# Kernel tuning notes

Hardware: AMD Instinct MI355X
Metric: run time of the kernel (lower is better)

Reference implementation:

```python
import jax, jax.numpy as jnp
import numpy as np

HEAD_SIZE = 128  # embeddings_dims // no_of_heads = 4096 // 32


def apply_rope(v):
    # v: [B, S, d] with d = HEAD_SIZE; interleaved-pair rotation as in source
    B, S, d = v.shape
    pos = jnp.arange(S, dtype=jnp.float32)[:, None]              # [S, 1]
    idx = jnp.arange(0, d, 2, dtype=jnp.float32)[None, :]        # [1, d//2]
    theta = jnp.power(10000.0, -2.0 * idx / d)                   # [1, d//2]
    angles = pos * theta                                         # [S, d//2]
    cos = jnp.cos(angles)
    sin = jnp.sin(angles)
    vr = v.reshape(B, S, d // 2, 2)
    x0, x1 = vr[..., 0], vr[..., 1]
    out = jnp.stack([x0 * cos - x1 * sin, x1 * cos + x0 * sin], axis=-1)
    return out.reshape(B, S, d)


def setup_inputs() -> dict:
    key = jax.random.key(0)
    kx, kq, kk, kv = jax.random.split(key, 4)
    B, S, D = 2, 4096, 4096
    d = HEAD_SIZE
    scale = 1.0 / np.sqrt(D)
    return {
        "x": jax.random.normal(kx, (B, S, D), dtype=jnp.float32),
        "Wq": jax.random.normal(kq, (d, D), dtype=jnp.float32) * scale,
        "Wk": jax.random.normal(kk, (d, D), dtype=jnp.float32) * scale,
        "Wv": jax.random.normal(kv, (d, D), dtype=jnp.float32) * scale,
    }


def reference(x, Wq, Wk, Wv):
    # single attention head, non-flash path (eval mode: dropout = identity)
    B, S, D = x.shape
    q = jnp.einsum('bsd,hd->bsh', x, Wq)  # [B, S, head]
    k = jnp.einsum('bsd,hd->bsh', x, Wk)
    v = jnp.einsum('bsd,hd->bsh', x, Wv)
    q = apply_rope(q)
    k = apply_rope(k)
    scale = k.shape[-1] ** (-0.5)
    scores = jnp.einsum('bqh,bkh->bqk', q, k) * scale  # [B, S, S]
    causal = jnp.tril(jnp.ones((S, S), dtype=bool))
    scores = jnp.where(causal, scores, -jnp.inf)
    weights = jax.nn.softmax(scores, axis=-1)
    out = jnp.einsum('bqk,bkh->bqh', weights, v)  # [B, S, head]
    return out
```

## Files before the change

### kernel.cpp

```cpp
#include <hip/hip_runtime.h>

typedef _Float16 half8 __attribute__((ext_vector_type(8)));
typedef _Float16 half2v __attribute__((ext_vector_type(2)));
typedef float f32x4 __attribute__((ext_vector_type(4)));

#define S_LEN 4096
#define D_DIM 4096
#define HD 128


#define ASTR 40
#define QSTR 136
__global__ __launch_bounds__(256) void proj_kernel(const float* __restrict__ x,
                                                   const float* __restrict__ wq,
                                                   const float* __restrict__ wk,
                                                   const float* __restrict__ wv,
                                                   _Float16* __restrict__ qw,
                                                   _Float16* __restrict__ kw,
                                                   _Float16* __restrict__ vt) {
    __shared__ __align__(16) _Float16 smem[128 * QSTR];
    _Float16* Ash = smem;
    _Float16* Bsh = smem + 128 * ASTR;
    const int tid = threadIdx.x;
    const int bx = blockIdx.x;
    const int M0 = blockIdx.y * 128;
    const float* w = (bx == 0) ? wq : (bx == 1) ? wk : wv;
    const int lane = tid & 63, wid = tid >> 6;
    const int wr = wid >> 1, wc = wid & 1;
    const int l15 = lane & 15, quad = lane >> 4;

    const int srow = tid >> 1, scol = (tid & 1) * 16;
    const float* xa = x + (size_t)(M0 + srow) * D_DIM + scol;
    const float* wb = w + (size_t)srow * D_DIM + scol;
    _Float16* ash = &Ash[srow * ASTR + scol];
    _Float16* bsh = &Bsh[srow * ASTR + scol];

    f32x4 acc[4][4];
    for (int mi = 0; mi < 4; ++mi)
        for (int ni = 0; ni < 4; ++ni)
            acc[mi][ni] = (f32x4){0.f, 0.f, 0.f, 0.f};

    float4 a0 = *(const float4*)(xa);
    float4 a1 = *(const float4*)(xa + 4);
    float4 a2 = *(const float4*)(xa + 8);
    float4 a3 = *(const float4*)(xa + 12);
    float4 b0 = *(const float4*)(wb);
    float4 b1 = *(const float4*)(wb + 4);
    float4 b2 = *(const float4*)(wb + 8);
    float4 b3 = *(const float4*)(wb + 12);

    for (int k0 = 0; k0 < D_DIM; k0 += 32) {
        half8 ha0 = { (_Float16)a0.x, (_Float16)a0.y, (_Float16)a0.z, (_Float16)a0.w,
                      (_Float16)a1.x, (_Float16)a1.y, (_Float16)a1.z, (_Float16)a1.w };
        half8 ha1 = { (_Float16)a2.x, (_Float16)a2.y, (_Float16)a2.z, (_Float16)a2.w,
                      (_Float16)a3.x, (_Float16)a3.y, (_Float16)a3.z, (_Float16)a3.w };
        half8 hb0 = { (_Float16)b0.x, (_Float16)b0.y, (_Float16)b0.z, (_Float16)b0.w,
                      (_Float16)b1.x, (_Float16)b1.y, (_Float16)b1.z, (_Float16)b1.w };
        half8 hb1 = { (_Float16)b2.x, (_Float16)b2.y, (_Float16)b2.z, (_Float16)b2.w,
                      (_Float16)b3.x, (_Float16)b3.y, (_Float16)b3.z, (_Float16)b3.w };
        *(half8*)ash = ha0;
        *(half8*)(ash + 8) = ha1;
        *(half8*)bsh = hb0;
        *(half8*)(bsh + 8) = hb1;
        __syncthreads();
        if (k0 + 32 < D_DIM) {
            a0 = *(const float4*)(xa + k0 + 32);
            a1 = *(const float4*)(xa + k0 + 36);
            a2 = *(const float4*)(xa + k0 + 40);
            a3 = *(const float4*)(xa + k0 + 44);
            b0 = *(const float4*)(wb + k0 + 32);
            b1 = *(const float4*)(wb + k0 + 36);
            b2 = *(const float4*)(wb + k0 + 40);
            b3 = *(const float4*)(wb + k0 + 44);
        }
        half8 af[4], bf[4];
        for (int mi = 0; mi < 4; ++mi)
            af[mi] = *(const half8*)&Ash[(wr * 64 + mi * 16 + l15) * ASTR + quad * 8];
        for (int ni = 0; ni < 4; ++ni)
            bf[ni] = *(const half8*)&Bsh[(wc * 64 + ni * 16 + l15) * ASTR + quad * 8];
        for (int mi = 0; mi < 4; ++mi)
            for (int ni = 0; ni < 4; ++ni)
                acc[mi][ni] = __builtin_amdgcn_mfma_f32_16x16x32_f16(af[mi], bf[ni],
                                                                     acc[mi][ni], 0, 0, 0);
        __syncthreads();
    }

    if (bx < 2) {
        for (int mi = 0; mi < 4; ++mi)
            for (int ni = 0; ni < 4; ++ni)
                for (int r = 0; r < 4; ++r)
                    smem[(wr * 64 + mi * 16 + quad * 4 + r) * QSTR +
                         wc * 64 + ni * 16 + l15] = (_Float16)acc[mi][ni][r];
        __syncthreads();
        _Float16* dst = ((bx == 0) ? qw : kw) + (size_t)M0 * HD;
        const int row = tid >> 1, c0 = (tid & 1) * 64;
        for (int j = 0; j < 8; ++j)
            *(half8*)&dst[row * HD + c0 + j * 8] = *(const half8*)&smem[row * QSTR + c0 + j * 8];
    } else {
        for (int mi = 0; mi < 4; ++mi)
            for (int ni = 0; ni < 4; ++ni)
                for (int r = 0; r < 4; ++r)
                    smem[(wc * 64 + ni * 16 + l15) * QSTR +
                         wr * 64 + mi * 16 + quad * 4 + r] = (_Float16)acc[mi][ni][r];
        __syncthreads();
        _Float16* dst = vt + (size_t)(M0 >> 12) * HD * S_LEN + (M0 & (S_LEN - 1));
        const int hd = tid >> 1, c0 = (tid & 1) * 64;
        for (int j = 0; j < 8; ++j)
            *(half8*)&dst[(size_t)hd * S_LEN + c0 + j * 8] =
                *(const half8*)&smem[hd * QSTR + c0 + j * 8];
    }
}

__global__ __launch_bounds__(256) void rope_kernel(_Float16* __restrict__ qw,
                                                   _Float16* __restrict__ kw) {
    const int g = blockIdx.x * 256 + threadIdx.x;
    const int m = g >> 6, p = g & 63;
    const int s = m & (S_LEN - 1);
    const float theta = exp2f((float)p * -0.4152410118609203f);
    float sn, cn;
    sincosf((float)s * theta, &sn, &cn);
    const size_t off = (size_t)m * HD + 2 * p;
    half2v qv = *(half2v*)&qw[off];
    half2v kv = *(half2v*)&kw[off];
    float q0 = qv[0], q1 = qv[1], k0 = kv[0], k1 = kv[1];
    half2v qo = { (_Float16)(q0 * cn - q1 * sn), (_Float16)(q1 * cn + q0 * sn) };
    half2v ko = { (_Float16)(k0 * cn - k1 * sn), (_Float16)(k1 * cn + k0 * sn) };
    *(half2v*)&qw[off] = qo;
    *(half2v*)&kw[off] = ko;
}

template<bool MASKED>
__device__ __forceinline__ void attn_tile(int kbase, int qg, int l15, int quad,
                                          const _Float16* __restrict__ kb,
                                          const _Float16* __restrict__ vtb,
                                          const half8* bq, f32x4* acc,
                                          float& mrun, float& lrun) {
    const float csc = 0.1275174348796053f;
    const _Float16* kr = kb + (size_t)(kbase + l15) * HD + quad * 8;
    f32x4 st0 = (f32x4){0.f, 0.f, 0.f, 0.f};
    f32x4 st1 = (f32x4){0.f, 0.f, 0.f, 0.f};
    for (int kk = 0; kk < 4; ++kk) {
        half8 k0 = *(const half8*)(kr + kk * 32);
        half8 k1 = *(const half8*)(kr + 16 * HD + kk * 32);
        st0 = __builtin_amdgcn_mfma_f32_16x16x32_f16(k0, bq[kk], st0, 0, 0, 0);
        st1 = __builtin_amdgcn_mfma_f32_16x16x32_f16(k1, bq[kk], st1, 0, 0, 0);
    }
    half8 va[8];
    const _Float16* vr = vtb + (size_t)l15 * S_LEN + kbase + quad * 8;
    for (int c = 0; c < 8; ++c)
        va[c] = *(const half8*)(vr + (size_t)c * 16 * S_LEN);
    float p0[4], p1[4];
    float mloc = -1e30f;
    for (int r = 0; r < 4; ++r) {
        float v0 = st0[r] * csc;
        float v1 = st1[r] * csc;
        if (MASKED) {
            const int key0 = kbase + quad * 4 + r;
            if (key0 > qg)      v0 = -1e30f;
            if (key0 + 16 > qg) v1 = -1e30f;
        }
        p0[r] = v0; p1[r] = v1;
        mloc = fmaxf(mloc, fmaxf(v0, v1));
    }
    mloc = fmaxf(mloc, __shfl_xor(mloc, 16));
    mloc = fmaxf(mloc, __shfl_xor(mloc, 32));
    const float mnew = fmaxf(mrun, mloc);
    const float alpha = exp2f(mrun - mnew);
    mrun = mnew;
    float ls = 0.f;
    for (int r = 0; r < 4; ++r) {
        p0[r] = exp2f(p0[r] - mnew);
        p1[r] = exp2f(p1[r] - mnew);
        ls += p0[r] + p1[r];
    }
    ls += __shfl_xor(ls, 16);
    ls += __shfl_xor(ls, 32);
    lrun = lrun * alpha + ls;
    for (int c = 0; c < 8; ++c)
        acc[c] *= alpha;
    int ph0 = __builtin_bit_cast(int, __builtin_amdgcn_cvt_pkrtz(p0[0], p0[1]));
    int ph1 = __builtin_bit_cast(int, __builtin_amdgcn_cvt_pkrtz(p0[2], p0[3]));
    int ph2 = __builtin_bit_cast(int, __builtin_amdgcn_cvt_pkrtz(p1[0], p1[1]));
    int ph3 = __builtin_bit_cast(int, __builtin_amdgcn_cvt_pkrtz(p1[2], p1[3]));
    const int s0 = (l15 + (((quad << 1)    ) & 3) * 16) * 4;
    const int s1 = (l15 + (((quad << 1) + 1) & 3) * 16) * 4;
    int a0 = __builtin_amdgcn_ds_bpermute(s0, ph0);
    int a1 = __builtin_amdgcn_ds_bpermute(s0, ph1);
    int a2 = __builtin_amdgcn_ds_bpermute(s1, ph0);
    int a3 = __builtin_amdgcn_ds_bpermute(s1, ph1);
    int b0 = __builtin_amdgcn_ds_bpermute(s0, ph2);
    int b1 = __builtin_amdgcn_ds_bpermute(s0, ph3);
    int b2 = __builtin_amdgcn_ds_bpermute(s1, ph2);
    int b3 = __builtin_amdgcn_ds_bpermute(s1, ph3);
    const bool lo = quad < 2;
    int4 pi = { lo ? a0 : b0, lo ? a1 : b1, lo ? a2 : b2, lo ? a3 : b3 };
    half8 pf = __builtin_bit_cast(half8, pi);
    for (int c = 0; c < 8; ++c)
        acc[c] = __builtin_amdgcn_mfma_f32_16x16x32_f16(va[c], pf, acc[c], 0, 0, 0);
}

__global__ __launch_bounds__(256) void attn_kernel(const _Float16* __restrict__ q,
                                                   const _Float16* __restrict__ k,
                                                   const _Float16* __restrict__ vt,
                                                   float* __restrict__ out) {
    __shared__ __align__(16) float Osh[4][16][132];
    __shared__ float msh[4][16];
    __shared__ float lsh[4][16];
    const int tid = threadIdx.x;
    const int lane = tid & 63, wv_ = tid >> 6;
    const int l15 = lane & 15, quad = lane >> 4;
    const int bidx = blockIdx.x;
    const int b = bidx & 1;
    const int t = 255 - (bidx >> 1);
    const int qb = t * 16;
    const int qg = qb + l15;

    const _Float16* qp = q + (size_t)(b * S_LEN + qb) * HD;
    half8 bq[4];
    for (int kk = 0; kk < 4; ++kk)
        bq[kk] = *(const half8*)&qp[l15 * HD + kk * 32 + quad * 8];

    f32x4 acc[8];
    for (int c = 0; c < 8; ++c) acc[c] = (f32x4){0.f, 0.f, 0.f, 0.f};
    float mrun = -1e30f, lrun = 0.f;

    const _Float16* kb = k + (size_t)b * S_LEN * HD;
    const _Float16* vtb = vt + (size_t)b * HD * S_LEN;

    const int nfull = (qb + 1) >> 5;
    for (int kt = wv_; kt < nfull; kt += 4)
        attn_tile<false>(kt * 32, qg, l15, quad, kb, vtb, bq, acc, mrun, lrun);
    if ((nfull & 3) == wv_)
        attn_tile<true>(nfull * 32, qg, l15, quad, kb, vtb, bq, acc, mrun, lrun);

    for (int c = 0; c < 8; ++c)
        *(f32x4*)&Osh[wv_][l15][c * 16 + quad * 4] = acc[c];
    if (quad == 0) { msh[wv_][l15] = mrun; lsh[wv_][l15] = lrun; }
    __syncthreads();

    const int qr = tid >> 4, dg = (tid & 15) * 8;
    float m0 = msh[0][qr], m1 = msh[1][qr], m2 = msh[2][qr], m3 = msh[3][qr];
    float mm = fmaxf(fmaxf(m0, m1), fmaxf(m2, m3));
    float f0 = exp2f(m0 - mm), f1 = exp2f(m1 - mm), f2 = exp2f(m2 - mm), f3 = exp2f(m3 - mm);
    float l = lsh[0][qr] * f0 + lsh[1][qr] * f1 + lsh[2][qr] * f2 + lsh[3][qr] * f3;
    f32x4 oa = (f32x4){0.f, 0.f, 0.f, 0.f}, ob = oa;
    oa += *(f32x4*)&Osh[0][qr][dg] * f0;  ob += *(f32x4*)&Osh[0][qr][dg + 4] * f0;
    oa += *(f32x4*)&Osh[1][qr][dg] * f1;  ob += *(f32x4*)&Osh[1][qr][dg + 4] * f1;
    oa += *(f32x4*)&Osh[2][qr][dg] * f2;  ob += *(f32x4*)&Osh[2][qr][dg + 4] * f2;
    oa += *(f32x4*)&Osh[3][qr][dg] * f3;  ob += *(f32x4*)&Osh[3][qr][dg + 4] * f3;
    const float inv = 1.0f / l;
    float* op = out + (size_t)(b * S_LEN + qb + qr) * HD + dg;
    *(float4*)op       = (float4){oa[0] * inv, oa[1] * inv, oa[2] * inv, oa[3] * inv};
    *(float4*)(op + 4) = (float4){ob[0] * inv, ob[1] * inv, ob[2] * inv, ob[3] * inv};
}

extern "C" void kernel_launch(void* const* d_in, const int* in_sizes, int n_in,
                              void* d_out, int out_size, void* d_ws, size_t ws_size,
                              hipStream_t stream) {
    const float* x  = (const float*)d_in[0];
    const float* Wq = (const float*)d_in[1];
    const float* Wk = (const float*)d_in[2];
    const float* Wv = (const float*)d_in[3];
    float* out = (float*)d_out;
    char* ws = (char*)d_ws;
    _Float16* qw = (_Float16*)(ws);
    _Float16* kw = (_Float16*)(ws + (2u << 20));
    _Float16* vt = (_Float16*)(ws + (4u << 20));

    proj_kernel<<<dim3(3, 64), dim3(256), 0, stream>>>(x, Wq, Wk, Wv, qw, kw, vt);
    rope_kernel<<<dim3(2048), dim3(256), 0, stream>>>(qw, kw);
    attn_kernel<<<dim3(512), dim3(256), 0, stream>>>(qw, kw, vt, out);
}
```

Baseline: 399.3 us.

## Halve projection M-tile, double-buffer its LDS, and prefetch K fragments in attention

```diff
diff --git a/kernel.cpp b/kernel.cpp
--- a/kernel.cpp
+++ b/kernel.cpp
@@ -18,96 +18,87 @@
                                                    _Float16* __restrict__ qw,
                                                    _Float16* __restrict__ kw,
                                                    _Float16* __restrict__ vt) {
-    __shared__ __align__(16) _Float16 smem[128 * QSTR];
-    _Float16* Ash = smem;
-    _Float16* Bsh = smem + 128 * ASTR;
+    __shared__ __align__(16) _Float16 smem[17408];
     const int tid = threadIdx.x;
     const int bx = blockIdx.x;
-    const int M0 = blockIdx.y * 128;
+    const int M0 = blockIdx.y * 64;
     const float* w = (bx == 0) ? wq : (bx == 1) ? wk : wv;
-    const int lane = tid & 63, wid = tid >> 6;
-    const int wr = wid >> 1, wc = wid & 1;
+    const int lane = tid & 63, wv_ = tid >> 6;
     const int l15 = lane & 15, quad = lane >> 4;
 
-    const int srow = tid >> 1, scol = (tid & 1) * 16;
-    const float* xa = x + (size_t)(M0 + srow) * D_DIM + scol;
-    const float* wb = w + (size_t)srow * D_DIM + scol;
-    _Float16* ash = &Ash[srow * ASTR + scol];
-    _Float16* bsh = &Bsh[srow * ASTR + scol];
-
-    f32x4 acc[4][4];
+    const int arow = tid >> 2, acol = (tid & 3) * 8;
+    const int brow = tid >> 1, bcol = (tid & 1) * 16;
+    const float* xa = x + (size_t)(M0 + arow) * D_DIM + acol;
+    const float* wb = w + (size_t)brow * D_DIM + bcol;
+
+    f32x4 acc[4][2];
     for (int mi = 0; mi < 4; ++mi)
-        for (int ni = 0; ni < 4; ++ni)
+        for (int ni = 0; ni < 2; ++ni)
             acc[mi][ni] = (f32x4){0.f, 0.f, 0.f, 0.f};
 
-    float4 a0 = *(const float4*)(xa);
-    float4 a1 = *(const float4*)(xa + 4);
-    float4 a2 = *(const float4*)(xa + 8);
-    float4 a3 = *(const float4*)(xa + 12);
-    float4 b0 = *(const float4*)(wb);
-    float4 b1 = *(const float4*)(wb + 4);
-    float4 b2 = *(const float4*)(wb + 8);
-    float4 b3 = *(const float4*)(wb + 12);
-
-    for (int k0 = 0; k0 < D_DIM; k0 += 32) {
-        half8 ha0 = { (_Float16)a0.x, (_Float16)a0.y, (_Float16)a0.z, (_Float16)a0.w,
-                      (_Float16)a1.x, (_Float16)a1.y, (_Float16)a1.z, (_Float16)a1.w };
-        half8 ha1 = { (_Float16)a2.x, (_Float16)a2.y, (_Float16)a2.z, (_Float16)a2.w,
-                      (_Float16)a3.x, (_Float16)a3.y, (_Float16)a3.z, (_Float16)a3.w };
-        half8 hb0 = { (_Float16)b0.x, (_Float16)b0.y, (_Float16)b0.z, (_Float16)b0.w,
-                      (_Float16)b1.x, (_Float16)b1.y, (_Float16)b1.z, (_Float16)b1.w };
-        half8 hb1 = { (_Float16)b2.x, (_Float16)b2.y, (_Float16)b2.z, (_Float16)b2.w,
-                      (_Float16)b3.x, (_Float16)b3.y, (_Float16)b3.z, (_Float16)b3.w };
-        *(half8*)ash = ha0;
-        *(half8*)(ash + 8) = ha1;
-        *(half8*)bsh = hb0;
-        *(half8*)(bsh + 8) = hb1;
+    float4 pa[2][2], pb[2][4];
+    pa[0][0] = *(const float4*)(xa);      pa[0][1] = *(const float4*)(xa + 4);
+    pb[0][0] = *(const float4*)(wb);      pb[0][1] = *(const float4*)(wb + 4);
+    pb[0][2] = *(const float4*)(wb + 8);  pb[0][3] = *(const float4*)(wb + 12);
+    pa[1][0] = *(const float4*)(xa + 32); pa[1][1] = *(const float4*)(xa + 36);
+    pb[1][0] = *(const float4*)(wb + 32); pb[1][1] = *(const float4*)(wb + 36);
+    pb[1][2] = *(const float4*)(wb + 40); pb[1][3] = *(const float4*)(wb + 44);
+
+    for (int i = 0; i < 128; ++i) {
+        const int p = i & 1;
+        _Float16* Ash = smem + p * 7680;
+        _Float16* Bsh = smem + p * 7680 + 2560;
+        half8 ha = { (_Float16)pa[p][0].x, (_Float16)pa[p][0].y, (_Float16)pa[p][0].z, (_Float16)pa[p][0].w,
+                     (_Float16)pa[p][1].x, (_Float16)pa[p][1].y, (_Float16)pa[p][1].z, (_Float16)pa[p][1].w };
+        half8 hb0 = { (_Float16)pb[p][0].x, (_Float16)pb[p][0].y, (_Float16)pb[p][0].z, (_Float16)pb[p][0].w,
+                      (_Float16)pb[p][1].x, (_Float16)pb[p][1].y, (_Float16)pb[p][1].z, (_Float16)pb[p][1].w };
+        half8 hb1 = { (_Float16)pb[p][2].x, (_Float16)pb[p][2].y, (_Float16)pb[p][2].z, (_Float16)pb[p][2].w,
+                      (_Float16)pb[p][3].x, (_Float16)pb[p][3].y, (_Float16)pb[p][3].z, (_Float16)pb[p][3].w };
+        *(half8*)&Ash[arow * ASTR + acol] = ha;
+        *(half8*)&Bsh[brow * ASTR + bcol] = hb0;
+        *(half8*)&Bsh[brow * ASTR + bcol + 8] = hb1;
+        if (i + 2 < 128) {
+            const int off = (i + 2) * 32;
+            pa[p][0] = *(const float4*)(xa + off);      pa[p][1] = *(const float4*)(xa + off + 4);
+            pb[p][0] = *(const float4*)(wb + off);      pb[p][1] = *(const float4*)(wb + off + 4);
+            pb[p][2] = *(const float4*)(wb + off + 8);  pb[p][3] = *(const float4*)(wb + off + 12);
+        }
         __syncthreads();
-        if (k0 + 32 < D_DIM) {
-            a0 = *(const float4*)(xa + k0 + 32);
-            a1 = *(const float4*)(xa + k0 + 36);
-            a2 = *(const float4*)(xa + k0 + 40);
-            a3 = *(const float4*)(xa + k0 + 44);
-            b0 = *(const float4*)(wb + k0 + 32);
-            b1 = *(const float4*)(wb + k0 + 36);
-            b2 = *(const float4*)(wb + k0 + 40);
-            b3 = *(const float4*)(wb + k0 + 44);
-        }
-        half8 af[4], bf[4];
-        for (int mi = 0; mi < 4; ++mi)
-            af[mi] = *(const half8*)&Ash[(wr * 64 + mi * 16 + l15) * ASTR + quad * 8];
-        for (int ni = 0; ni < 4; ++ni)
-            bf[ni] = *(const half8*)&Bsh[(wc * 64 + ni * 16 + l15) * ASTR + quad * 8];
-        for (int mi = 0; mi < 4; ++mi)
-            for (int ni = 0; ni < 4; ++ni)
+        half8 af[4], bf[2];
+        for (int mi = 0; mi < 4; ++mi)
+            af[mi] = *(const half8*)&Ash[(mi * 16 + l15) * ASTR + quad * 8];
+        for (int ni = 0; ni < 2; ++ni)
+            bf[ni] = *(const half8*)&Bsh[(wv_ * 32 + ni * 16 + l15) * ASTR + quad * 8];
+        for (int mi = 0; mi < 4; ++mi)
+            for (int ni = 0; ni < 2; ++ni)
                 acc[mi][ni] = __builtin_amdgcn_mfma_f32_16x16x32_f16(af[mi], bf[ni],
                                                                      acc[mi][ni], 0, 0, 0);
-        __syncthreads();
-    }
+    }
+    __syncthreads();
 
     if (bx < 2) {
         for (int mi = 0; mi < 4; ++mi)
-            for (int ni = 0; ni < 4; ++ni)
+            for (int ni = 0; ni < 2; ++ni)
                 for (int r = 0; r < 4; ++r)
-                    smem[(wr * 64 + mi * 16 + quad * 4 + r) * QSTR +
-                         wc * 64 + ni * 16 + l15] = (_Float16)acc[mi][ni][r];
+                    smem[(mi * 16 + quad * 4 + r) * QSTR + wv_ * 32 + ni * 16 + l15] =
+                        (_Float16)acc[mi][ni][r];
         __syncthreads();
         _Float16* dst = ((bx == 0) ? qw : kw) + (size_t)M0 * HD;
-        const int row = tid >> 1, c0 = (tid & 1) * 64;
-        for (int j = 0; j < 8; ++j)
+        const int row = tid >> 2, c0 = (tid & 3) * 32;
+        for (int j = 0; j < 4; ++j)
             *(half8*)&dst[row * HD + c0 + j * 8] = *(const half8*)&smem[row * QSTR + c0 + j * 8];
     } else {
         for (int mi = 0; mi < 4; ++mi)
-            for (int ni = 0; ni < 4; ++ni)
+            for (int ni = 0; ni < 2; ++ni)
                 for (int r = 0; r < 4; ++r)
-                    smem[(wc * 64 + ni * 16 + l15) * QSTR +
-                         wr * 64 + mi * 16 + quad * 4 + r] = (_Float16)acc[mi][ni][r];
+                    smem[(wv_ * 32 + ni * 16 + l15) * QSTR + mi * 16 + quad * 4 + r] =
+                        (_Float16)acc[mi][ni][r];
         __syncthreads();
         _Float16* dst = vt + (size_t)(M0 >> 12) * HD * S_LEN + (M0 & (S_LEN - 1));
-        const int hd = tid >> 1, c0 = (tid & 1) * 64;
-        for (int j = 0; j < 8; ++j)
-            *(half8*)&dst[(size_t)hd * S_LEN + c0 + j * 8] =
-                *(const half8*)&smem[hd * QSTR + c0 + j * 8];
+        const int hd = tid >> 1, s0 = (tid & 1) * 32;
+        for (int j = 0; j < 4; ++j)
+            *(half8*)&dst[(size_t)hd * S_LEN + s0 + j * 8] =
+                *(const half8*)&smem[hd * QSTR + s0 + j * 8];
     }
 }
 
@@ -129,21 +120,27 @@
     *(half2v*)&kw[off] = ko;
 }
 
+__device__ __forceinline__ void load_kf(const _Float16* __restrict__ kb, int kbase,
+                                        int l15, int quad, half8* kf) {
+    const _Float16* kr = kb + (size_t)(kbase + l15) * HD + quad * 8;
+    for (int kk = 0; kk < 4; ++kk) {
+        kf[kk]     = *(const half8*)(kr + kk * 32);
+        kf[4 + kk] = *(const half8*)(kr + 16 * HD + kk * 32);
+    }
+}
+
 template<bool MASKED>
 __device__ __forceinline__ void attn_tile(int kbase, int qg, int l15, int quad,
-                                          const _Float16* __restrict__ kb,
+                                          const half8* kf,
                                           const _Float16* __restrict__ vtb,
                                           const half8* bq, f32x4* acc,
                                           float& mrun, float& lrun) {
     const float csc = 0.1275174348796053f;
-    const _Float16* kr = kb + (size_t)(kbase + l15) * HD + quad * 8;
     f32x4 st0 = (f32x4){0.f, 0.f, 0.f, 0.f};
     f32x4 st1 = (f32x4){0.f, 0.f, 0.f, 0.f};
     for (int kk = 0; kk < 4; ++kk) {
-        half8 k0 = *(const half8*)(kr + kk * 32);
-        half8 k1 = *(const half8*)(kr + 16 * HD + kk * 32);
-        st0 = __builtin_amdgcn_mfma_f32_16x16x32_f16(k0, bq[kk], st0, 0, 0, 0);
-        st1 = __builtin_amdgcn_mfma_f32_16x16x32_f16(k1, bq[kk], st1, 0, 0, 0);
+        st0 = __builtin_amdgcn_mfma_f32_16x16x32_f16(kf[kk],     bq[kk], st0, 0, 0, 0);
+        st1 = __builtin_amdgcn_mfma_f32_16x16x32_f16(kf[4 + kk], bq[kk], st1, 0, 0, 0);
     }
     half8 va[8];
     const _Float16* vr = vtb + (size_t)l15 * S_LEN + kbase + quad * 8;
@@ -228,10 +225,22 @@
     const _Float16* vtb = vt + (size_t)b * HD * S_LEN;
 
     const int nfull = (qb + 1) >> 5;
-    for (int kt = wv_; kt < nfull; kt += 4)
-        attn_tile<false>(kt * 32, qg, l15, quad, kb, vtb, bq, acc, mrun, lrun);
-    if ((nfull & 3) == wv_)
-        attn_tile<true>(nfull * 32, qg, l15, quad, kb, vtb, bq, acc, mrun, lrun);
+    const int kend = nfull * 32;
+    const bool hasm = ((nfull & 3) == wv_);
+    const int kb0 = wv_ * 32;
+
+    half8 kf[8], kf2[8];
+    if (kb0 < kend)      load_kf(kb, kb0, l15, quad, kf);
+    else if (hasm)       load_kf(kb, kend, l15, quad, kf);
+    for (int kbase = kb0; kbase < kend; kbase += 128) {
+        const int kn = kbase + 128;
+        if (kn < kend)   load_kf(kb, kn, l15, quad, kf2);
+        else if (hasm)   load_kf(kb, kend, l15, quad, kf2);
+        attn_tile<false>(kbase, qg, l15, quad, kf, vtb, bq, acc, mrun, lrun);
+        for (int j = 0; j < 8; ++j) kf[j] = kf2[j];
+    }
+    if (hasm)
+        attn_tile<true>(kend, qg, l15, quad, kf, vtb, bq, acc, mrun, lrun);
 
     for (int c = 0; c < 8; ++c)
         *(f32x4*)&Osh[wv_][l15][c * 16 + quad * 4] = acc[c];
@@ -267,7 +276,7 @@
     _Float16* kw = (_Float16*)(ws + (2u << 20));
     _Float16* vt = (_Float16*)(ws + (4u << 20));
 
-    proj_kernel<<<dim3(3, 64), dim3(256), 0, stream>>>(x, Wq, Wk, Wv, qw, kw, vt);
+    proj_kernel<<<dim3(3, 128), dim3(256), 0, stream>>>(x, Wq, Wk, Wv, qw, kw, vt);
     rope_kernel<<<dim3(2048), dim3(256), 0, stream>>>(qw, kw);
     attn_kernel<<<dim3(512), dim3(256), 0, stream>>>(qw, kw, vt, out);
 }
```

After: 747.9 us. 1.87x slower.
